# Performance work log

Measured on AMD Instinct MI355X. Metric: run time of the kernel, lower is better.

## Reference

```python
import jax, jax.numpy as jnp
import numpy as np

N, E = 20000, 200000
HID, NH, L = 128, 8, 7
DH = HID // NH
SCALE = float(np.sqrt(DH))
NNUM = 5
MLP_IN = HID + HID + 8 + 8 + 8 + NNUM  # 285
EPS = 1e-5


def _ln(x, g, b):
    mu = jnp.mean(x, -1, keepdims=True)
    var = jnp.mean((x - mu) ** 2, -1, keepdims=True)
    return (x - mu) * jax.lax.rsqrt(var + EPS) * g + b


def setup_inputs() -> dict:
    key = jax.random.key(0)
    ks = jax.random.split(key, 24)
    f = lambda k, s: (0.05 * jax.random.normal(k, s)).astype(jnp.float32)
    z = lambda s: jnp.zeros(s, jnp.float32)
    o = lambda s: jnp.ones(s, jnp.float32)
    inp = {
        'node_feats': f(ks[0], (N, 2)),
        'numericals': f(ks[1], (E, NNUM)),
        'W_emb': f(ks[2], (2, HID)), 'b_emb': z((HID,)),
        'WQ': f(ks[3], (L, HID, HID)), 'bQ': z((L, HID)),
        'WK': f(ks[4], (L, HID, HID)), 'bK': z((L, HID)),
        'WV': f(ks[5], (L, HID, HID)), 'bV': z((L, HID)),
        'WO': f(ks[6], (L, HID, HID)), 'bO': z((L, HID)),
        'ln1_g': o((L, HID)), 'ln1_b': z((L, HID)),
        'ln2_g': o((L, HID)), 'ln2_b': z((L, HID)),
        'W1': f(ks[7], (L, HID, HID)), 'b1': z((L, HID)),
        'W2': f(ks[8], (L, HID, HID)), 'b2': z((L, HID)),
        'curr_emb': f(ks[9], (15, 8)), 'pay_emb': f(ks[10], (7, 8)),
        'mlp_Wh': f(ks[11], (3, MLP_IN, MLP_IN)), 'mlp_bh': z((3, MLP_IN)),
        'mlp_Wo': f(ks[12], (MLP_IN, 2)), 'mlp_bo': z((2,)),
        'src': jax.random.randint(ks[13], (E,), 0, N, dtype=jnp.int32),
        'dst': jax.random.randint(ks[14], (E,), 0, N, dtype=jnp.int32),
        'payment_currency': jax.random.randint(ks[15], (E,), 0, 15, dtype=jnp.int32),
        'receiving_currency': jax.random.randint(ks[16], (E,), 0, 15, dtype=jnp.int32),
        'payment_format': jax.random.randint(ks[17], (E,), 0, 7, dtype=jnp.int32),
    }
    return inp


def reference(node_feats, numericals, W_emb, b_emb, WQ, bQ, WK, bK, WV, bV, WO, bO,
              ln1_g, ln1_b, ln2_g, ln2_b, W1, b1, W2, b2, curr_emb, pay_emb,
              mlp_Wh, mlp_bh, mlp_Wo, mlp_bo, src, dst,
              payment_currency, receiving_currency, payment_format):
    h = node_feats @ W_emb + b_emb  # [N, HID]
    for l in range(L):
        # --- graph multi-head attention (segment softmax over in-edges of dst) ---
        x = _ln(h, ln1_g[l], ln1_b[l])
        Q = (x @ WQ[l] + bQ[l]).reshape(N, NH, DH)
        K = (x @ WK[l] + bK[l]).reshape(N, NH, DH)
        V = (x @ WV[l] + bV[l]).reshape(N, NH, DH)
        scores = jnp.einsum('ehd,ehd->eh', Q[dst], K[src]) / SCALE  # [E, NH]
        m = jax.ops.segment_max(scores, dst, num_segments=N)        # [N, NH]
        ex = jnp.exp(scores - m[dst])
        den = jax.ops.segment_sum(ex, dst, num_segments=N)
        w = ex / den[dst]                                           # attn weights per edge
        attn = jax.ops.segment_sum(w[:, :, None] * V[src], dst, num_segments=N)
        h = h + attn.reshape(N, HID) @ WO[l] + bO[l]
        # --- FFN ---
        x = _ln(h, ln2_g[l], ln2_b[l])
        h = h + jax.nn.relu(x @ W1[l] + b1[l]) @ W2[l] + b2[l]
    # --- edge classifier ---
    ef = jnp.concatenate([curr_emb[payment_currency], curr_emb[receiving_currency],
                          pay_emb[payment_format], numericals], axis=1)  # [E, 29]
    y = jnp.concatenate([h[src], h[dst], ef], axis=1)  # [E, 285]
    for i in range(3):
        y = jax.nn.relu(y @ mlp_Wh[i] + mlp_bh[i])
    return y @ mlp_Wo + mlp_bo  # [E, 2]
```

## Files before the change

### kernel.cpp

```cpp
#include <hip/hip_runtime.h>

#define HID 128
#define NH 8
#define DH 16
#define NLAYERS 7
#define MLP_IN 285
#define MP 288
#define LDW 296
#define XS 136

typedef short short8 __attribute__((ext_vector_type(8)));
typedef float f32x4 __attribute__((ext_vector_type(4)));
typedef float f32x16 __attribute__((ext_vector_type(16)));
typedef unsigned short ushort8 __attribute__((ext_vector_type(8)));

__device__ inline unsigned short f2bf(float f) {
    union { float f; unsigned int u; } v; v.f = f;
    unsigned int r = v.u + 0x7FFF + ((v.u >> 16) & 1);
    return (unsigned short)(r >> 16);
}
__device__ inline float bf2f(unsigned short u) {
    union { unsigned int u; float f; } v; v.u = ((unsigned int)u) << 16;
    return v.f;
}

__global__ __launch_bounds__(256) void embed_kernel(
    const float* __restrict__ nf, const float* __restrict__ We,
    const float* __restrict__ be, float* __restrict__ h, int N)
{
    int idx = blockIdx.x * 256 + threadIdx.x;
    if (idx >= N * HID) return;
    int n = idx >> 7, j = idx & 127;
    h[idx] = fmaf(nf[n * 2], We[j], fmaf(nf[n * 2 + 1], We[HID + j], be[j]));
}

__global__ __launch_bounds__(256) void prep_nodew_kernel(
    const float* __restrict__ WQ, const float* __restrict__ WK,
    const float* __restrict__ WV, const float* __restrict__ WO,
    const float* __restrict__ W1, const float* __restrict__ W2,
    unsigned short* __restrict__ wnh, unsigned short* __restrict__ wnl)
{
    int idx = blockIdx.x * 256 + threadIdx.x;
    if (idx >= 42 * 32 * 64) return;
    int lane = idx & 63;
    int r = idx >> 6;
    int kt = r & 7; r >>= 3;
    int ct = r & 3; r >>= 2;
    int m = r;
    int l = m / 6, wi = m - l * 6;
    const float* Wb;
    switch (wi) {
        case 0: Wb = WQ; break; case 1: Wb = WK; break; case 2: Wb = WV; break;
        case 3: Wb = WO; break; case 4: Wb = W1; break; default: Wb = W2; break;
    }
    Wb += (size_t)l * HID * HID;
    int n = ct * 32 + (lane & 31);
    int kb = kt * 16 + (lane >> 5) * 8;
    ushort8 vh, vl;
#pragma unroll
    for (int j = 0; j < 8; ++j) {
        float w = Wb[(size_t)(kb + j) * HID + n];
        unsigned short hi = f2bf(w);
        vh[j] = hi;
        vl[j] = f2bf(w - bf2f(hi));
    }
    *(ushort8*)&wnh[(size_t)idx * 8] = vh;
    *(ushort8*)&wnl[(size_t)idx * 8] = vl;
}

#define LOADB(m, BH, BL) do { \
    size_t fb_ = (((size_t)(matbase + (m)) * 32 + (size_t)wave * 8) * 64 + lane) * 8; \
    const unsigned short* Bh_ = wnh + fb_; \
    const unsigned short* Bl_ = wnl + fb_; \
    _Pragma("unroll") \
    for (int kt = 0; kt < 8; ++kt) { \
        BH[kt] = *(const short8*)&Bh_[kt * 512]; \
        BL[kt] = *(const short8*)&Bl_[kt * 512]; \
    } \
} while (0)

#define COMPSTORE(BH, BL, BIAS, OUT, STRIDE, OFF) do { \
    f32x16 acc = {}; \
    _Pragma("unroll") \
    for (int kt = 0; kt < 8; ++kt) \
        acc = __builtin_amdgcn_mfma_f32_32x32x16_bf16(ah[kt], BH[kt], acc, 0, 0, 0); \
    _Pragma("unroll") \
    for (int kt = 0; kt < 8; ++kt) \
        acc = __builtin_amdgcn_mfma_f32_32x32x16_bf16(al[kt], BH[kt], acc, 0, 0, 0); \
    _Pragma("unroll") \
    for (int kt = 0; kt < 8; ++kt) \
        acc = __builtin_amdgcn_mfma_f32_32x32x16_bf16(ah[kt], BL[kt], acc, 0, 0, 0); \
    int col_ = wave * 32 + l31; \
    float bv_ = (BIAS)[col_]; \
    _Pragma("unroll") \
    for (int r = 0; r < 16; ++r) { \
        int rowm_ = (r & 3) + 8 * (r >> 2) + 4 * half; \
        int row_ = rowBase + rowm_; \
        if (row_ < M) (OUT)[(size_t)row_ * (STRIDE) + (OFF) + col_] = acc[r] + bv_; \
    } \
} while (0)

__global__ __launch_bounds__(256, 2) void ln_qkv_mfma(
    const float* __restrict__ h,
    const float* __restrict__ g, const float* __restrict__ bb,
    const unsigned short* __restrict__ wnh, const unsigned short* __restrict__ wnl,
    int matbase,
    const float* __restrict__ bQ, const float* __restrict__ bK, const float* __restrict__ bV,
    float* __restrict__ qo, float* __restrict__ kvo, int M)
{
    __shared__ unsigned short Xh[32][XS];
    __shared__ unsigned short Xl[32][XS];
    int tid = threadIdx.x;
    int lane = tid & 63, wave = tid >> 6;
    int rowBase = blockIdx.x * 32;

    for (int i = 0; i < 8; ++i) {
        int r = wave * 8 + i;
        int row = rowBase + r;
        float a0 = 0.f, a1 = 0.f;
        if (row < M) {
            a0 = h[(size_t)row * HID + lane];
            a1 = h[(size_t)row * HID + 64 + lane];
        }
        float s = a0 + a1;
#pragma unroll
        for (int off = 32; off > 0; off >>= 1) s += __shfl_down(s, off, 64);
        s = __shfl(s, 0, 64);
        float mu = s * (1.0f / 128.0f);
        float d0 = a0 - mu, d1 = a1 - mu;
        float v = d0 * d0 + d1 * d1;
#pragma unroll
        for (int off = 32; off > 0; off >>= 1) v += __shfl_down(v, off, 64);
        v = __shfl(v, 0, 64);
        float rr = rsqrtf(v * (1.0f / 128.0f) + 1e-5f);
        float x0 = d0 * rr * g[lane] + bb[lane];
        float x1 = d1 * rr * g[64 + lane] + bb[64 + lane];
        unsigned short h0 = f2bf(x0), h1 = f2bf(x1);
        Xh[r][lane] = h0;           Xh[r][64 + lane] = h1;
        Xl[r][lane] = f2bf(x0 - bf2f(h0));
        Xl[r][64 + lane] = f2bf(x1 - bf2f(h1));
    }
    __syncthreads();

    int l31 = lane & 31;
    int half = lane >> 5;

    short8 ah[8], al[8];
#pragma unroll
    for (int kt = 0; kt < 8; ++kt) {
        ah[kt] = *(const short8*)&Xh[l31][kt * 16 + half * 8];
        al[kt] = *(const short8*)&Xl[l31][kt * 16 + half * 8];
    }

    short8 bh0[8], bl0[8], bh1[8], bl1[8];
    LOADB(0, bh0, bl0);
    LOADB(1, bh1, bl1);
    COMPSTORE(bh0, bl0, bQ, qo, HID, 0);
    LOADB(2, bh0, bl0);
    COMPSTORE(bh1, bl1, bK, kvo, 256, 0);
    COMPSTORE(bh0, bl0, bV, kvo, 256, 128);
}

__global__ __launch_bounds__(256, 2) void post_mfma(
    const float* __restrict__ at, const float* __restrict__ hin,
    const unsigned short* __restrict__ wnh, const unsigned short* __restrict__ wnl,
    int matbase,
    const float* __restrict__ bO,
    const float* __restrict__ g2, const float* __restrict__ b2g,
    const float* __restrict__ b1, const float* __restrict__ b2,
    float* __restrict__ hout, int M)
{
    __shared__ unsigned short Ah[32][XS];
    __shared__ unsigned short Al[32][XS];
    __shared__ unsigned short Th[32][XS];
    __shared__ unsigned short Tl[32][XS];
    __shared__ float Hs[32][132];
    int tid = threadIdx.x;
    int lane = tid & 63, wave = tid >> 6;
    int rowBase = blockIdx.x * 32;
    int l31 = lane & 31;
    int half = lane >> 5;

    for (int i = tid; i < 32 * 32; i += 256) {
        int r = i >> 5, c4 = i & 31;
        int row = rowBase + r;
        float4 va = make_float4(0.f, 0.f, 0.f, 0.f), vh = va;
        if (row < M) {
            va = *(const float4*)&at[(size_t)row * HID + c4 * 4];
            vh = *(const float4*)&hin[(size_t)row * HID + c4 * 4];
        }
        const float* vp = (const float*)&va;
#pragma unroll
        for (int q = 0; q < 4; ++q) {
            unsigned short hi = f2bf(vp[q]);
            Ah[r][c4 * 4 + q] = hi;
            Al[r][c4 * 4 + q] = f2bf(vp[q] - bf2f(hi));
        }
        *(float4*)&Hs[r][c4 * 4] = vh;
    }
    __syncthreads();

    int colW = wave * 32 + l31;

    {
        short8 ah[8], al[8];
#pragma unroll
        for (int kt = 0; kt < 8; ++kt) {
            ah[kt] = *(const short8*)&Ah[l31][kt * 16 + half * 8];
            al[kt] = *(const short8*)&Al[l31][kt * 16 + half * 8];
        }
        short8 bh[8], bl[8];
        {
            size_t fb = (((size_t)(matbase + 3) * 32 + (size_t)wave * 8) * 64 + lane) * 8;
            const unsigned short* Bh = wnh + fb;
            const unsigned short* Bl = wnl + fb;
#pragma unroll
            for (int kt = 0; kt < 8; ++kt) {
                bh[kt] = *(const short8*)&Bh[kt * 512];
                bl[kt] = *(const short8*)&Bl[kt * 512];
            }
        }
        f32x16 acc = {};
#pragma unroll
        for (int kt = 0; kt < 8; ++kt)
            acc = __builtin_amdgcn_mfma_f32_32x32x16_bf16(ah[kt], bh[kt], acc, 0, 0, 0);
#pragma unroll
        for (int kt = 0; kt < 8; ++kt)
            acc = __builtin_amdgcn_mfma_f32_32x32x16_bf16(al[kt], bh[kt], acc, 0, 0, 0);
#pragma unroll
        for (int kt = 0; kt < 8; ++kt)
            acc = __builtin_amdgcn_mfma_f32_32x32x16_bf16(ah[kt], bl[kt], acc, 0, 0, 0);
        float bv = bO[colW];
#pragma unroll
        for (int r = 0; r < 16; ++r) {
            int rowm = (r & 3) + 8 * (r >> 2) + 4 * half;
            Hs[rowm][colW] += acc[r] + bv;
        }
    }
    __syncthreads();

    for (int i = 0; i < 8; ++i) {
        int r = wave * 8 + i;
        float a0 = Hs[r][lane];
        float a1 = Hs[r][64 + lane];
        float s = a0 + a1;
#pragma unroll
        for (int off = 32; off > 0; off >>= 1) s += __shfl_down(s, off, 64);
        s = __shfl(s, 0, 64);
        float mu = s * (1.0f / 128.0f);
        float d0 = a0 - mu, d1 = a1 - mu;
        float v = d0 * d0 + d1 * d1;
#pragma unroll
        for (int off = 32; off > 0; off >>= 1) v += __shfl_down(v, off, 64);
        v = __shfl(v, 0, 64);
        float rr = rsqrtf(v * (1.0f / 128.0f) + 1e-5f);
        float x0 = d0 * rr * g2[lane] + b2g[lane];
        float x1 = d1 * rr * g2[64 + lane] + b2g[64 + lane];
        unsigned short h0 = f2bf(x0), h1 = f2bf(x1);
        Ah[r][lane] = h0;           Ah[r][64 + lane] = h1;
        Al[r][lane] = f2bf(x0 - bf2f(h0));
        Al[r][64 + lane] = f2bf(x1 - bf2f(h1));
    }
    __syncthreads();

    {
        short8 ah[8], al[8];
#pragma unroll
        for (int kt = 0; kt < 8; ++kt) {
            ah[kt] = *(const short8*)&Ah[l31][kt * 16 + half * 8];
            al[kt] = *(const short8*)&Al[l31][kt * 16 + half * 8];
        }
        short8 bh[8], bl[8];
        {
            size_t fb = (((size_t)(matbase + 4) * 32 + (size_t)wave * 8) * 64 + lane) * 8;
            const unsigned short* Bh = wnh + fb;
            const unsigned short* Bl = wnl + fb;
#pragma unroll
            for (int kt = 0; kt < 8; ++kt) {
                bh[kt] = *(const short8*)&Bh[kt * 512];
                bl[kt] = *(const short8*)&Bl[kt * 512];
            }
        }
        f32x16 acc = {};
#pragma unroll
        for (int kt = 0; kt < 8; ++kt)
            acc = __builtin_amdgcn_mfma_f32_32x32x16_bf16(ah[kt], bh[kt], acc, 0, 0, 0);
#pragma unroll
        for (int kt = 0; kt < 8; ++kt)
            acc = __builtin_amdgcn_mfma_f32_32x32x16_bf16(al[kt], bh[kt], acc, 0, 0, 0);
#pragma unroll
        for (int kt = 0; kt < 8; ++kt)
            acc = __builtin_amdgcn_mfma_f32_32x32x16_bf16(ah[kt], bl[kt], acc, 0, 0, 0);
        float bv = b1[colW];
#pragma unroll
        for (int r = 0; r < 16; ++r) {
            int rowm = (r & 3) + 8 * (r >> 2) + 4 * half;
            float t = fmaxf(acc[r] + bv, 0.f);
            unsigned short hi = f2bf(t);
            Th[rowm][colW] = hi;
            Tl[rowm][colW] = f2bf(t - bf2f(hi));
        }
    }
    __syncthreads();

    {
        short8 ah[8], al[8];
#pragma unroll
        for (int kt = 0; kt < 8; ++kt) {
            ah[kt] = *(const short8*)&Th[l31][kt * 16 + half * 8];
            al[kt] = *(const short8*)&Tl[l31][kt * 16 + half * 8];
        }
        short8 bh[8], bl[8];
        {
            size_t fb = (((size_t)(matbase + 5) * 32 + (size_t)wave * 8) * 64 + lane) * 8;
            const unsigned short* Bh = wnh + fb;
            const unsigned short* Bl = wnl + fb;
#pragma unroll
            for (int kt = 0; kt < 8; ++kt) {
                bh[kt] = *(const short8*)&Bh[kt * 512];
                bl[kt] = *(const short8*)&Bl[kt * 512];
            }
        }
        f32x16 acc = {};
#pragma unroll
        for (int kt = 0; kt < 8; ++kt)
            acc = __builtin_amdgcn_mfma_f32_32x32x16_bf16(ah[kt], bh[kt], acc, 0, 0, 0);
#pragma unroll
        for (int kt = 0; kt < 8; ++kt)
            acc = __builtin_amdgcn_mfma_f32_32x32x16_bf16(al[kt], bh[kt], acc, 0, 0, 0);
#pragma unroll
        for (int kt = 0; kt < 8; ++kt)
            acc = __builtin_amdgcn_mfma_f32_32x32x16_bf16(ah[kt], bl[kt], acc, 0, 0, 0);
        float bv = b2[colW];
#pragma unroll
        for (int r = 0; r < 16; ++r) {
            int rowm = (r & 3) + 8 * (r >> 2) + 4 * half;
            int row = rowBase + rowm;
            if (row < M)
                hout[(size_t)row * HID + colW] = Hs[rowm][colW] + acc[r] + bv;
        }
    }
}

__global__ __launch_bounds__(256) void deg_kernel(
    const int* __restrict__ dst, int* __restrict__ deg, int E)
{
    int e = blockIdx.x * 256 + threadIdx.x;
    if (e < E) atomicAdd(&deg[dst[e]], 1);
}

__global__ __launch_bounds__(256) void scan_kernel(
    const int* __restrict__ deg, int* __restrict__ rowptr,
    int* __restrict__ cursor, int N)
{
    __shared__ int sums[256];
    int tid = threadIdx.x;
    int chunk = (N + 255) / 256;
    int lo = tid * chunk;
    int hi = lo + chunk; if (hi > N) hi = N;
    int s = 0;
    for (int i = lo; i < hi && i >= 0; ++i) s += deg[i];
    sums[tid] = s;
    __syncthreads();
    for (int off = 1; off < 256; off <<= 1) {
        int v = (tid >= off) ? sums[tid - off] : 0;
        __syncthreads();
        sums[tid] += v;
        __syncthreads();
    }
    int base = (tid == 0) ? 0 : sums[tid - 1];
    for (int i = lo; i < hi; ++i) {
        rowptr[i] = base; cursor[i] = base; base += deg[i];
    }
    if (tid == 255) rowptr[N] = sums[255];
}

__global__ __launch_bounds__(256) void scatter_kernel(
    const int* __restrict__ src, const int* __restrict__ dst,
    int* __restrict__ cursor, int* __restrict__ ssrc, int E)
{
    int e = blockIdx.x * 256 + threadIdx.x;
    if (e < E) {
        int p = atomicAdd(&cursor[dst[e]], 1);
        ssrc[p] = src[e];
    }
}

__global__ __launch_bounds__(256) void attn_fused_kernel(
    const float* __restrict__ q, const float* __restrict__ kv,
    const int* __restrict__ rowptr, const int* __restrict__ ssrc,
    float* __restrict__ at, int N)
{
    int node = blockIdx.x * 4 + (threadIdx.x >> 6);
    int lane = threadIdx.x & 63;
    if (node >= N) return;
    int beg = rowptr[node], end = rowptr[node + 1];
    float q0 = q[(size_t)node * HID + lane];
    float q1 = q[(size_t)node * HID + 64 + lane];
    float acc0 = 0.f, acc1 = 0.f, den0 = 0.f, den1 = 0.f;
    int i = beg;
    for (; i + 2 <= end; i += 2) {
        int s0 = ssrc[i], s1 = ssrc[i + 1];
        const float* kv0 = kv + (size_t)s0 * 256;
        const float* kv1 = kv + (size_t)s1 * 256;
        float k00 = kv0[lane],       k01 = kv0[64 + lane];
        float v00 = kv0[128 + lane], v01 = kv0[192 + lane];
        float k10 = kv1[lane],       k11 = kv1[64 + lane];
        float v10 = kv1[128 + lane], v11 = kv1[192 + lane];
        float p00 = q0 * k00, p01 = q1 * k01;
        float p10 = q0 * k10, p11 = q1 * k11;
#pragma unroll
        for (int off = 1; off < 16; off <<= 1) {
            p00 += __shfl_xor(p00, off, 64);
            p01 += __shfl_xor(p01, off, 64);
            p10 += __shfl_xor(p10, off, 64);
            p11 += __shfl_xor(p11, off, 64);
        }
        float w00 = __expf(p00 * 0.25f), w01 = __expf(p01 * 0.25f);
        float w10 = __expf(p10 * 0.25f), w11 = __expf(p11 * 0.25f);
        den0 += w00 + w10; den1 += w01 + w11;
        acc0 = fmaf(w10, v10, fmaf(w00, v00, acc0));
        acc1 = fmaf(w11, v11, fmaf(w01, v01, acc1));
    }
    if (i < end) {
        int s = ssrc[i];
        const float* kv0 = kv + (size_t)s * 256;
        float k0 = kv0[lane], k1 = kv0[64 + lane];
        float p0 = q0 * k0, p1 = q1 * k1;
#pragma unroll
        for (int off = 1; off < 16; off <<= 1) {
            p0 += __shfl_xor(p0, off, 64);
            p1 += __shfl_xor(p1, off, 64);
        }
        float w0 = __expf(p0 * 0.25f), w1 = __expf(p1 * 0.25f);
        den0 += w0; den1 += w1;
        acc0 = fmaf(w0, kv0[128 + lane], acc0);
        acc1 = fmaf(w1, kv0[192 + lane], acc1);
    }
    at[(size_t)node * HID + lane]      = (den0 > 0.f) ? acc0 / den0 : 0.f;
    at[(size_t)node * HID + 64 + lane] = (den1 > 0.f) ? acc1 / den1 : 0.f;
}

__global__ __launch_bounds__(256) void prep_wp_kernel(
    const float* __restrict__ Wh, unsigned short* __restrict__ wp)
{
    int idx = blockIdx.x * 256 + threadIdx.x;
    if (idx >= 3 * 9 * 18 * 64) return;
    int lane = idx & 63;
    int r = idx >> 6;
    int kt = r % 18; r /= 18;
    int ct = r % 9;
    int layer = r / 9;
    int n = ct * 32 + (lane & 31);
    int kbase = kt * 16 + (lane >> 5) * 8;
    ushort8 val;
#pragma unroll
    for (int j = 0; j < 8; ++j) {
        int k = kbase + j;
        float v = (n < MLP_IN && k < MLP_IN)
            ? Wh[(size_t)layer * MLP_IN * MLP_IN + (size_t)k * MLP_IN + n] : 0.f;
        val[j] = f2bf(v);
    }
    *(ushort8*)&wp[(size_t)idx * 8] = val;
}

__global__ __launch_bounds__(256) void prep_hb_kernel(
    const float* __restrict__ h, unsigned short* __restrict__ hb, int n)
{
    int idx = blockIdx.x * 256 + threadIdx.x;
    if (idx >= n) return;
    hb[idx] = f2bf(h[idx]);
}

__global__ __launch_bounds__(256, 4) void edge_mlp_mfma(
    const unsigned short* __restrict__ hb, const float* __restrict__ ce,
    const float* __restrict__ pe, const float* __restrict__ num,
    const int* __restrict__ src, const int* __restrict__ dst,
    const int* __restrict__ pc, const int* __restrict__ rc,
    const int* __restrict__ pf,
    const unsigned short* __restrict__ wp, const float* __restrict__ bh,
    const float* __restrict__ Wo, const float* __restrict__ bo,
    float* __restrict__ out, int E)
{
    __shared__ unsigned short y[64 * LDW];
    int tid = threadIdx.x;
    int e0 = blockIdx.x * 64;
    int wave = tid >> 6;
    int lane = tid & 63;
    int l31 = lane & 31;
    int half = lane >> 5;

    for (int i = tid; i < 64 * 36; i += 256) {
        int t = i / 36;
        int c = i - t * 36;
        int e = e0 + t;
        if (e >= E) e = E - 1;
        ushort8 val;
        if (c < 16) {
            val = *(const ushort8*)&hb[(size_t)src[e] * HID + c * 8];
        } else if (c < 32) {
            val = *(const ushort8*)&hb[(size_t)dst[e] * HID + (c - 16) * 8];
        } else if (c == 32) {
            const float* p = &ce[pc[e] * 8];
#pragma unroll
            for (int j = 0; j < 8; ++j) val[j] = f2bf(p[j]);
        } else if (c == 33) {
            const float* p = &ce[rc[e] * 8];
#pragma unroll
            for (int j = 0; j < 8; ++j) val[j] = f2bf(p[j]);
        } else if (c == 34) {
            const float* p = &pe[pf[e] * 8];
#pragma unroll
            for (int j = 0; j < 8; ++j) val[j] = f2bf(p[j]);
        } else {
            const float* p = &num[(size_t)e * 5];
#pragma unroll
            for (int j = 0; j < 5; ++j) val[j] = f2bf(p[j]);
            val[5] = 0; val[6] = 0; val[7] = 0;
        }
        *(ushort8*)&y[t * LDW + c * 8] = val;
    }
    __syncthreads();

    int slab = wave >> 1;
    int rowA = slab * 32 + l31;
    int ctlo = (wave & 1) ? 5 : 0;
    int cthi = (wave & 1) ? 9 : 5;

    for (int layer = 0; layer < 3; ++layer) {
        const float* __restrict__ bias = bh + layer * MLP_IN;

        short8 afr[18];
#pragma unroll
        for (int kt = 0; kt < 18; ++kt)
            afr[kt] = *(const short8*)&y[rowA * LDW + kt * 16 + half * 8];
        __syncthreads();

        for (int ct = ctlo; ct < cthi; ++ct) {
            const unsigned short* __restrict__ Bp =
                wp + (size_t)layer * 82944 + (size_t)ct * 9216 + (size_t)lane * 8;
            short8 bfr[18];
#pragma unroll
            for (int kt = 0; kt < 18; ++kt)
                bfr[kt] = *(const short8*)&Bp[kt * 512];
            f32x16 acc = {};
#pragma unroll
            for (int kt = 0; kt < 18; ++kt)
                acc = __builtin_amdgcn_mfma_f32_32x32x16_bf16(afr[kt], bfr[kt], acc, 0, 0, 0);
            int col = ct * 32 + l31;
            if (col < MLP_IN) {
                float bv = bias[col];
#pragma unroll
                for (int r = 0; r < 16; ++r) {
                    int rowm = (r & 3) + 8 * (r >> 2) + 4 * half;
                    float t = fmaxf(acc[r] + bv, 0.f);
                    y[(slab * 32 + rowm) * LDW + col] = f2bf(t);
                }
            }
        }
        __syncthreads();
    }

    {
        int t = tid >> 2;
        int oc = tid & 1;
        int kk = (tid >> 1) & 1;
        int e = e0 + t;
        const unsigned short* yr = &y[t * LDW];
        float p0 = 0.f, p1 = 0.f, p2 = 0.f, p3 = 0.f;
        int kc_lo = kk ? 18 : 0;
        int kc_hi = kk ? 35 : 18;
        for (int kc = kc_lo; kc < kc_hi; ++kc) {
            ushort8 yv = *(const ushort8*)&yr[kc * 8];
            int kb = kc * 8;
            p0 = fmaf(bf2f(yv[0]), Wo[(kb + 0) * 2 + oc], p0);
            p1 = fmaf(bf2f(yv[1]), Wo[(kb + 1) * 2 + oc], p1);
            p2 = fmaf(bf2f(yv[2]), Wo[(kb + 2) * 2 + oc], p2);
            p3 = fmaf(bf2f(yv[3]), Wo[(kb + 3) * 2 + oc], p3);
            p0 = fmaf(bf2f(yv[4]), Wo[(kb + 4) * 2 + oc], p0);
            p1 = fmaf(bf2f(yv[5]), Wo[(kb + 5) * 2 + oc], p1);
            p2 = fmaf(bf2f(yv[6]), Wo[(kb + 6) * 2 + oc], p2);
            p3 = fmaf(bf2f(yv[7]), Wo[(kb + 7) * 2 + oc], p3);
        }
        float acc = (p0 + p1) + (p2 + p3);
        if (kk) {
            for (int k = 280; k < MLP_IN; ++k)
                acc = fmaf(bf2f(yr[k]), Wo[k * 2 + oc], acc);
        }
        acc += __shfl_xor(acc, 2, 64);
        if (kk == 0 && e < E)
            out[(size_t)e * 2 + oc] = acc + bo[oc];
    }
}

extern "C" void kernel_launch(void* const* d_in, const int* in_sizes, int n_in,
                              void* d_out, int out_size, void* d_ws, size_t ws_size,
                              hipStream_t stream)
{
    const float* node_feats = (const float*)d_in[0];
    const float* numericals = (const float*)d_in[1];
    const float* W_emb = (const float*)d_in[2];
    const float* b_emb = (const float*)d_in[3];
    const float* WQ = (const float*)d_in[4];
    const float* bQ = (const float*)d_in[5];
    const float* WK = (const float*)d_in[6];
    const float* bK = (const float*)d_in[7];
    const float* WV = (const float*)d_in[8];
    const float* bV = (const float*)d_in[9];
    const float* WO = (const float*)d_in[10];
    const float* bO = (const float*)d_in[11];
    const float* ln1_g = (const float*)d_in[12];
    const float* ln1_b = (const float*)d_in[13];
    const float* ln2_g = (const float*)d_in[14];
    const float* ln2_b = (const float*)d_in[15];
    const float* W1 = (const float*)d_in[16];
    const float* b1 = (const float*)d_in[17];
    const float* W2 = (const float*)d_in[18];
    const float* b2 = (const float*)d_in[19];
    const float* curr_emb = (const float*)d_in[20];
    const float* pay_emb = (const float*)d_in[21];
    const float* mlp_Wh = (const float*)d_in[22];
    const float* mlp_bh = (const float*)d_in[23];
    const float* mlp_Wo = (const float*)d_in[24];
    const float* mlp_bo = (const float*)d_in[25];
    const int* src = (const int*)d_in[26];
    const int* dst = (const int*)d_in[27];
    const int* pc = (const int*)d_in[28];
    const int* rc = (const int*)d_in[29];
    const int* pf = (const int*)d_in[30];

    const int N = in_sizes[0] / 2;
    const int E = in_sizes[26];

    float* ws = (float*)d_ws;
    float* h   = ws;
    float* qb  = h   + (size_t)N * HID;
    float* kvb = qb  + (size_t)N * HID;
    float* at  = kvb + (size_t)N * HID * 2;
    unsigned short* hb = (unsigned short*)(at + (size_t)N * HID);
    unsigned short* wpk = hb + (size_t)N * HID;
    unsigned short* wnh = wpk + (size_t)3 * 9 * 18 * 64 * 8;
    unsigned short* wnl = wnh + (size_t)42 * 32 * 64 * 8;
    int* rowptr = (int*)(wnl + (size_t)42 * 32 * 64 * 8);
    int* deg    = rowptr + (N + 1);
    int* cursor = deg + N;
    int* ssrc   = cursor + N;

    prep_wp_kernel<<<(3 * 9 * 18 * 64 + 255) / 256, 256, 0, stream>>>(mlp_Wh, wpk);
    prep_nodew_kernel<<<(42 * 32 * 64 + 255) / 256, 256, 0, stream>>>(
        WQ, WK, WV, WO, W1, W2, wnh, wnl);

    embed_kernel<<<(N * HID + 255) / 256, 256, 0, stream>>>(node_feats, W_emb, b_emb, h, N);

    hipMemsetAsync(deg, 0, (size_t)N * sizeof(int), stream);
    deg_kernel<<<(E + 255) / 256, 256, 0, stream>>>(dst, deg, E);
    scan_kernel<<<1, 256, 0, stream>>>(deg, rowptr, cursor, N);
    scatter_kernel<<<(E + 255) / 256, 256, 0, stream>>>(src, dst, cursor, ssrc, E);

    int nodeBlocks = (N + 31) / 32;

    for (int l = 0; l < NLAYERS; ++l) {
        ln_qkv_mfma<<<nodeBlocks, 256, 0, stream>>>(
            h, ln1_g + l * HID, ln1_b + l * HID,
            wnh, wnl, l * 6,
            bQ + l * HID, bK + l * HID, bV + l * HID,
            qb, kvb, N);

        attn_fused_kernel<<<(N + 3) / 4, 256, 0, stream>>>(qb, kvb, rowptr, ssrc, at, N);

        post_mfma<<<nodeBlocks, 256, 0, stream>>>(
            at, h, wnh, wnl, l * 6,
            bO + l * HID,
            ln2_g + l * HID, ln2_b + l * HID,
            b1 + l * HID, b2 + l * HID,
            h, N);
    }

    prep_hb_kernel<<<(N * HID + 255) / 256, 256, 0, stream>>>(h, hb, N * HID);

    edge_mlp_mfma<<<(E + 63) / 64, 256, 0, stream>>>(
        hb, curr_emb, pay_emb, numericals, src, dst, pc, rc, pf,
        wpk, mlp_bh, mlp_Wo, mlp_bo, (float*)d_out, E);
}
```

Baseline: 1.041 ms.

## Fuse attention, post-MLP and next-layer LN+QKV into one per-layer kernel

Merges the edge-attention gather, the output projection plus FFN, and the next layer's LayerNorm plus QKV projection into a single kernel per layer, with double-buffered Q/KV buffers so the next layer's projections do not overwrite the ones still being read. The last layer writes the bf16 copy of h directly, which removes the separate conversion kernel. This cuts kernel launches and the global round trips for the attention output and h. In exchange, attention now runs at one wave per node, 8 nodes per wave inside 32-row blocks limited to 2 blocks per SM, so the latency-bound gather may get less parallelism.

```diff
diff --git a/kernel.cpp b/kernel.cpp
--- a/kernel.cpp
+++ b/kernel.cpp
@@ -161,14 +161,21 @@
     COMPSTORE(bh0, bl0, bV, kvo, 256, 128);
 }
 
-__global__ __launch_bounds__(256, 2) void post_mfma(
-    const float* __restrict__ at, const float* __restrict__ hin,
+__global__ __launch_bounds__(256, 2) void attn_post_qkv(
+    const float* __restrict__ qin, const float* __restrict__ kvin,
+    const int* __restrict__ rowptr, const int* __restrict__ ssrc,
     const unsigned short* __restrict__ wnh, const unsigned short* __restrict__ wnl,
     int matbase,
     const float* __restrict__ bO,
     const float* __restrict__ g2, const float* __restrict__ b2g,
     const float* __restrict__ b1, const float* __restrict__ b2,
-    float* __restrict__ hout, int M)
+    float* __restrict__ h,
+    int doQkv,
+    const float* __restrict__ g1n, const float* __restrict__ b1n,
+    const float* __restrict__ bQn, const float* __restrict__ bKn, const float* __restrict__ bVn,
+    float* __restrict__ qout, float* __restrict__ kvout,
+    unsigned short* __restrict__ hbout,
+    int M)
 {
     __shared__ unsigned short Ah[32][XS];
     __shared__ unsigned short Al[32][XS];
@@ -181,22 +188,64 @@
     int l31 = lane & 31;
     int half = lane >> 5;
 
-    for (int i = tid; i < 32 * 32; i += 256) {
-        int r = i >> 5, c4 = i & 31;
-        int row = rowBase + r;
-        float4 va = make_float4(0.f, 0.f, 0.f, 0.f), vh = va;
-        if (row < M) {
-            va = *(const float4*)&at[(size_t)row * HID + c4 * 4];
-            vh = *(const float4*)&hin[(size_t)row * HID + c4 * 4];
-        }
-        const float* vp = (const float*)&va;
-#pragma unroll
-        for (int q = 0; q < 4; ++q) {
-            unsigned short hi = f2bf(vp[q]);
-            Ah[r][c4 * 4 + q] = hi;
-            Al[r][c4 * 4 + q] = f2bf(vp[q] - bf2f(hi));
-        }
-        *(float4*)&Hs[r][c4 * 4] = vh;
+    for (int i = 0; i < 8; ++i) {
+        int r = wave * 8 + i;
+        int node = rowBase + r;
+        float hv0 = 0.f, hv1 = 0.f, a0 = 0.f, a1 = 0.f;
+        if (node < M) {
+            hv0 = h[(size_t)node * HID + lane];
+            hv1 = h[(size_t)node * HID + 64 + lane];
+            int beg = rowptr[node], end = rowptr[node + 1];
+            float q0 = qin[(size_t)node * HID + lane];
+            float q1 = qin[(size_t)node * HID + 64 + lane];
+            float acc0 = 0.f, acc1 = 0.f, den0 = 0.f, den1 = 0.f;
+            int e = beg;
+            for (; e + 2 <= end; e += 2) {
+                int s0 = ssrc[e], s1 = ssrc[e + 1];
+                const float* kv0 = kvin + (size_t)s0 * 256;
+                const float* kv1 = kvin + (size_t)s1 * 256;
+                float k00 = kv0[lane],       k01 = kv0[64 + lane];
+                float v00 = kv0[128 + lane], v01 = kv0[192 + lane];
+                float k10 = kv1[lane],       k11 = kv1[64 + lane];
+                float v10 = kv1[128 + lane], v11 = kv1[192 + lane];
+                float p00 = q0 * k00, p01 = q1 * k01;
+                float p10 = q0 * k10, p11 = q1 * k11;
+#pragma unroll
+                for (int off = 1; off < 16; off <<= 1) {
+                    p00 += __shfl_xor(p00, off, 64);
+                    p01 += __shfl_xor(p01, off, 64);
+                    p10 += __shfl_xor(p10, off, 64);
+                    p11 += __shfl_xor(p11, off, 64);
+                }
+                float w00 = __expf(p00 * 0.25f), w01 = __expf(p01 * 0.25f);
+                float w10 = __expf(p10 * 0.25f), w11 = __expf(p11 * 0.25f);
+                den0 += w00 + w10; den1 += w01 + w11;
+                acc0 = fmaf(w10, v10, fmaf(w00, v00, acc0));
+                acc1 = fmaf(w11, v11, fmaf(w01, v01, acc1));
+            }
+            if (e < end) {
+                int s = ssrc[e];
+                const float* kv0 = kvin + (size_t)s * 256;
+                float k0 = kv0[lane], k1 = kv0[64 + lane];
+                float p0 = q0 * k0, p1 = q1 * k1;
+#pragma unroll
+                for (int off = 1; off < 16; off <<= 1) {
+                    p0 += __shfl_xor(p0, off, 64);
+                    p1 += __shfl_xor(p1, off, 64);
+                }
+                float w0 = __expf(p0 * 0.25f), w1 = __expf(p1 * 0.25f);
+                den0 += w0; den1 += w1;
+                acc0 = fmaf(w0, kv0[128 + lane], acc0);
+                acc1 = fmaf(w1, kv0[192 + lane], acc1);
+            }
+            a0 = (den0 > 0.f) ? acc0 / den0 : 0.f;
+            a1 = (den1 > 0.f) ? acc1 / den1 : 0.f;
+        }
+        Hs[r][lane] = hv0;           Hs[r][64 + lane] = hv1;
+        unsigned short u0 = f2bf(a0), u1 = f2bf(a1);
+        Ah[r][lane] = u0;            Ah[r][64 + lane] = u1;
+        Al[r][lane] = f2bf(a0 - bf2f(u0));
+        Al[r][64 + lane] = f2bf(a1 - bf2f(u1));
     }
     __syncthreads();
 
@@ -336,9 +385,56 @@
         for (int r = 0; r < 16; ++r) {
             int rowm = (r & 3) + 8 * (r >> 2) + 4 * half;
             int row = rowBase + rowm;
-            if (row < M)
-                hout[(size_t)row * HID + colW] = Hs[rowm][colW] + acc[r] + bv;
-        }
+            float hn = Hs[rowm][colW] + acc[r] + bv;
+            Hs[rowm][colW] = hn;
+            if (row < M) {
+                if (doQkv) h[(size_t)row * HID + colW] = hn;
+                else       hbout[(size_t)row * HID + colW] = f2bf(hn);
+            }
+        }
+    }
+
+    if (!doQkv) return;
+    __syncthreads();
+
+    for (int i = 0; i < 8; ++i) {
+        int r = wave * 8 + i;
+        float a0 = Hs[r][lane];
+        float a1 = Hs[r][64 + lane];
+        float s = a0 + a1;
+#pragma unroll
+        for (int off = 32; off > 0; off >>= 1) s += __shfl_down(s, off, 64);
+        s = __shfl(s, 0, 64);
+        float mu = s * (1.0f / 128.0f);
+        float d0 = a0 - mu, d1 = a1 - mu;
+        float v = d0 * d0 + d1 * d1;
+#pragma unroll
+        for (int off = 32; off > 0; off >>= 1) v += __shfl_down(v, off, 64);
+        v = __shfl(v, 0, 64);
+        float rr = rsqrtf(v * (1.0f / 128.0f) + 1e-5f);
+        float x0 = d0 * rr * g1n[lane] + b1n[lane];
+        float x1 = d1 * rr * g1n[64 + lane] + b1n[64 + lane];
+        unsigned short h0 = f2bf(x0), h1 = f2bf(x1);
+        Ah[r][lane] = h0;           Ah[r][64 + lane] = h1;
+        Al[r][lane] = f2bf(x0 - bf2f(h0));
+        Al[r][64 + lane] = f2bf(x1 - bf2f(h1));
+    }
+    __syncthreads();
+
+    {
+        short8 ah[8], al[8];
+#pragma unroll
+        for (int kt = 0; kt < 8; ++kt) {
+            ah[kt] = *(const short8*)&Ah[l31][kt * 16 + half * 8];
+            al[kt] = *(const short8*)&Al[l31][kt * 16 + half * 8];
+        }
+        short8 bh0[8], bl0[8], bh1[8], bl1[8];
+        LOADB(6, bh0, bl0);
+        LOADB(7, bh1, bl1);
+        COMPSTORE(bh0, bl0, bQn, qout, HID, 0);
+        LOADB(8, bh0, bl0);
+        COMPSTORE(bh1, bl1, bKn, kvout, 256, 0);
+        COMPSTORE(bh0, bl0, bVn, kvout, 256, 128);
     }
 }
 
@@ -384,61 +480,6 @@
         int p = atomicAdd(&cursor[dst[e]], 1);
         ssrc[p] = src[e];
     }
-}
-
-__global__ __launch_bounds__(256) void attn_fused_kernel(
-    const float* __restrict__ q, const float* __restrict__ kv,
-    const int* __restrict__ rowptr, const int* __restrict__ ssrc,
-    float* __restrict__ at, int N)
-{
-    int node = blockIdx.x * 4 + (threadIdx.x >> 6);
-    int lane = threadIdx.x & 63;
-    if (node >= N) return;
-    int beg = rowptr[node], end = rowptr[node + 1];
-    float q0 = q[(size_t)node * HID + lane];
-    float q1 = q[(size_t)node * HID + 64 + lane];
-    float acc0 = 0.f, acc1 = 0.f, den0 = 0.f, den1 = 0.f;
-    int i = beg;
-    for (; i + 2 <= end; i += 2) {
-        int s0 = ssrc[i], s1 = ssrc[i + 1];
-        const float* kv0 = kv + (size_t)s0 * 256;
-        const float* kv1 = kv + (size_t)s1 * 256;
-        float k00 = kv0[lane],       k01 = kv0[64 + lane];
-        float v00 = kv0[128 + lane], v01 = kv0[192 + lane];
-        float k10 = kv1[lane],       k11 = kv1[64 + lane];
-        float v10 = kv1[128 + lane], v11 = kv1[192 + lane];
-        float p00 = q0 * k00, p01 = q1 * k01;
-        float p10 = q0 * k10, p11 = q1 * k11;
-#pragma unroll
-        for (int off = 1; off < 16; off <<= 1) {
-            p00 += __shfl_xor(p00, off, 64);
-            p01 += __shfl_xor(p01, off, 64);
-            p10 += __shfl_xor(p10, off, 64);
-            p11 += __shfl_xor(p11, off, 64);
-        }
-        float w00 = __expf(p00 * 0.25f), w01 = __expf(p01 * 0.25f);
-        float w10 = __expf(p10 * 0.25f), w11 = __expf(p11 * 0.25f);
-        den0 += w00 + w10; den1 += w01 + w11;
-        acc0 = fmaf(w10, v10, fmaf(w00, v00, acc0));
-        acc1 = fmaf(w11, v11, fmaf(w01, v01, acc1));
-    }
-    if (i < end) {
-        int s = ssrc[i];
-        const float* kv0 = kv + (size_t)s * 256;
-        float k0 = kv0[lane], k1 = kv0[64 + lane];
-        float p0 = q0 * k0, p1 = q1 * k1;
-#pragma unroll
-        for (int off = 1; off < 16; off <<= 1) {
-            p0 += __shfl_xor(p0, off, 64);
-            p1 += __shfl_xor(p1, off, 64);
-        }
-        float w0 = __expf(p0 * 0.25f), w1 = __expf(p1 * 0.25f);
-        den0 += w0; den1 += w1;
-        acc0 = fmaf(w0, kv0[128 + lane], acc0);
-        acc1 = fmaf(w1, kv0[192 + lane], acc1);
-    }
-    at[(size_t)node * HID + lane]      = (den0 > 0.f) ? acc0 / den0 : 0.f;
-    at[(size_t)node * HID + 64 + lane] = (den1 > 0.f) ? acc1 / den1 : 0.f;
 }
 
 __global__ __launch_bounds__(256) void prep_wp_kernel(
@@ -462,14 +503,6 @@
         val[j] = f2bf(v);
     }
     *(ushort8*)&wp[(size_t)idx * 8] = val;
-}
-
-__global__ __launch_bounds__(256) void prep_hb_kernel(
-    const float* __restrict__ h, unsigned short* __restrict__ hb, int n)
-{
-    int idx = blockIdx.x * 256 + threadIdx.x;
-    if (idx >= n) return;
-    hb[idx] = f2bf(h[idx]);
 }
 
 __global__ __launch_bounds__(256, 4) void edge_mlp_mfma(
@@ -633,11 +666,12 @@
     const int E = in_sizes[26];
 
     float* ws = (float*)d_ws;
-    float* h   = ws;
-    float* qb  = h   + (size_t)N * HID;
-    float* kvb = qb  + (size_t)N * HID;
-    float* at  = kvb + (size_t)N * HID * 2;
-    unsigned short* hb = (unsigned short*)(at + (size_t)N * HID);
+    float* h    = ws;
+    float* qb0  = h    + (size_t)N * HID;
+    float* kvb0 = qb0  + (size_t)N * HID;
+    float* qb1  = kvb0 + (size_t)N * HID * 2;
+    float* kvb1 = qb1  + (size_t)N * HID;
+    unsigned short* hb = (unsigned short*)(kvb1 + (size_t)N * HID * 2);
     unsigned short* wpk = hb + (size_t)N * HID;
     unsigned short* wnh = wpk + (size_t)3 * 9 * 18 * 64 * 8;
     unsigned short* wnl = wnh + (size_t)42 * 32 * 64 * 8;
@@ -659,24 +693,29 @@
 
     int nodeBlocks = (N + 31) / 32;
 
+    ln_qkv_mfma<<<nodeBlocks, 256, 0, stream>>>(
+        h, ln1_g, ln1_b, wnh, wnl, 0,
+        bQ, bK, bV, qb0, kvb0, N);
+
+    float* qbuf[2]  = { qb0, qb1 };
+    float* kvbuf[2] = { kvb0, kvb1 };
+
     for (int l = 0; l < NLAYERS; ++l) {
-        ln_qkv_mfma<<<nodeBlocks, 256, 0, stream>>>(
-            h, ln1_g + l * HID, ln1_b + l * HID,
+        int cur = l & 1, nxt = cur ^ 1;
+        int doQkv = (l < NLAYERS - 1) ? 1 : 0;
+        int ln = (l + 1 < NLAYERS) ? (l + 1) : 0;
+        attn_post_qkv<<<nodeBlocks, 256, 0, stream>>>(
+            qbuf[cur], kvbuf[cur], rowptr, ssrc,
             wnh, wnl, l * 6,
-            bQ + l * HID, bK + l * HID, bV + l * HID,
-            qb, kvb, N);
-
-        attn_fused_kernel<<<(N + 3) / 4, 256, 0, stream>>>(qb, kvb, rowptr, ssrc, at, N);
-
-        post_mfma<<<nodeBlocks, 256, 0, stream>>>(
-            at, h, wnh, wnl, l * 6,
             bO + l * HID,
             ln2_g + l * HID, ln2_b + l * HID,
             b1 + l * HID, b2 + l * HID,
-            h, N);
-    }
-
-    prep_hb_kernel<<<(N * HID + 255) / 256, 256, 0, stream>>>(h, hb, N * HID);
+            h, doQkv,
+            ln1_g + ln * HID, ln1_b + ln * HID,
+            bQ + ln * HID, bK + ln * HID, bV + ln * HID,
+            qbuf[nxt], kvbuf[nxt],
+            hb, N);
+    }
 
     edge_mlp_mfma<<<(E + 63) / 64, 256, 0, stream>>>(
         hb, curr_emb, pay_emb, numericals, src, dst, pc, rc, pf,
```

Result: slower. 1.299 ms (+24.8%).
